# Kernel tuning notes

Hardware: AMD Instinct MI355X
Metric: run time of the kernel (lower is better)

## Reference

```python
import jax, jax.numpy as jnp
import numpy as np

ALPHA = 0.5
MOM = 0.9            # momentum m in the recurrence
ACTIVATION = "tanh"
NUM_LAYERS = 2
CACHE = 32           # GROUP size
NK = 4               # n_kernel_feats
B, N, E = 4, 4096, 128


def _act(T):
    if ACTIVATION == "leaky-relu":
        return jax.nn.leaky_relu(T)
    elif ACTIVATION == "tanh":
        return jnp.tanh(T)
    return T


def _group_indices(N, cache, stage):
    # vectorized group_pos_to_index_v2 over all (group_nr, pos_in_group)
    m = N // cache
    o = np.arange(cache)
    s = 0 if stage == 0 else (1 << (stage - 1)) % m
    g = np.arange(m)[:, None]
    block = (g + o[None, :] * s) % m
    return jnp.asarray(block * cache + o[None, :])  # [m, cache], a permutation of 0..N-1


def _ncn_layer(X, Xa, W, stage):
    B, N, E = X.shape
    ce = E // NK
    m = N // CACHE
    idx = _group_indices(N, CACHE, stage)           # [m, cache]
    Wi = W[:E].reshape(NK, ce)
    Wj = W[E:].reshape(NK, ce)
    # gather groups: [B, m, NK, cache, ce]
    xg = jnp.moveaxis(X.reshape(B, N, NK, ce)[:, idx], 3, 2)
    xag = jnp.moveaxis(Xa.reshape(B, N, NK, ce)[:, idx], 3, 2)

    def step(carry, j):
        xi, xa = carry                               # [B, m, NK, cache, ce]
        xj = jnp.take(xi, j, axis=3)                 # [B, m, NK, ce]  (row start_j)
        sim = (jnp.einsum('bgnke,ne->bgnk', xi, Wi)
               + jnp.einsum('bgne,ne->bgn', xj, Wj)[..., None])   # [B, m, NK, cache]
        T = ALPHA * xi + (1.0 - ALPHA) * sim[..., None] * xj[:, :, :, None, :]
        F = _act(T)
        ya = MOM * xa + (1.0 - MOM) * F
        yi = MOM * xi + (1.0 - MOM) * ya
        return (yi, ya), None

    (yi, ya), _ = jax.lax.scan(step, (xg, xag), jnp.arange(CACHE))

    # scatter back; idx is a permutation so .set reproduces the += into zeros
    def scatter(v):
        v = jnp.moveaxis(v, 2, 3).reshape(B, m * CACHE, E)
        return jnp.zeros((B, N, E), v.dtype).at[:, idx.reshape(-1)].set(v)

    return scatter(yi), scatter(ya)


def setup_inputs() -> dict:
    key = jax.random.key(0)
    k1, k2, k3 = jax.random.split(key, 3)
    x = jax.random.normal(k1, (B, N, E), jnp.float32)
    xa = jax.random.normal(k2, (B, N, E), jnp.float32)
    W = jax.random.normal(k3, (NUM_LAYERS, 2 * E), jnp.float32)
    return {"x": x, "xa": xa, "W": W}


def reference(x, xa, W):
    for l in range(NUM_LAYERS):
        x, xa = _ncn_layer(x, xa, W[l], l)
    return x, xa
```

## Files before the change

kernel.cpp:

```cpp
#include <hip/hip_runtime.h>


namespace {
constexpr int kB = 4;
constexpr int kN = 4096;
constexpr int kE = 128;
constexpr int kCE = 32;
constexpr int kF  = 8;
constexpr int kQ  = kF / 2;
constexpr int kCache = 32;
constexpr int kM = kN / kCache;

typedef __attribute__((ext_vector_type(2))) float f32x2;

__device__ __forceinline__ f32x2 pk_fma(f32x2 a, f32x2 b, f32x2 c) {
    return __builtin_elementwise_fma(a, b, c);
}
}

__global__ void __launch_bounds__(128) ncn_layer_kernel(
    const float* __restrict__ x_in, const float* __restrict__ xa_in,
    const float* __restrict__ Wl,
    float* __restrict__ x_out, float* __restrict__ xa_out,
    int s)
{
    const int blk = blockIdx.x;
    const int n   = blk & 3;
    const int g   = (blk >> 2) & (kM - 1);
    const int b   = blk >> 9;
    const int t   = threadIdx.x;
    const int w   = t >> 6;
    const int l   = t & 63;
    const int orr = l >> 2;
    const int f   = l & 3;
    const int row = w * 16 + orr;

    const int r = (((g + row * s) & (kM - 1)) << 5) + row;
    const size_t base = ((size_t)(b * kN + r)) * kE + n * kCE + f * kF;

    constexpr float L1 = 1.4426950408889634f;

    f32x2 xi[kQ], xa[kQ], wi[kQ], wj[kQ];

    {
        const float4* xi4 = reinterpret_cast<const float4*>(x_in + base);
        const float4* xa4 = reinterpret_cast<const float4*>(xa_in + base);
        const float4* wi4 = reinterpret_cast<const float4*>(Wl + n * kCE + f * kF);
        const float4* wj4 = reinterpret_cast<const float4*>(Wl + kE + n * kCE + f * kF);
#pragma unroll
        for (int q = 0; q < kQ / 2; ++q) {
            float4 v = xi4[q];
            xi[2 * q + 0] = f32x2{v.x, v.y}; xi[2 * q + 1] = f32x2{v.z, v.w};
            float4 a = xa4[q];
            xa[2 * q + 0] = f32x2{a.x, a.y}; xa[2 * q + 1] = f32x2{a.z, a.w};
            float4 u = wi4[q];
            wi[2 * q + 0] = f32x2{u.x * L1, u.y * L1};
            wi[2 * q + 1] = f32x2{u.z * L1, u.w * L1};
            float4 ww = wj4[q];
            wj[2 * q + 0] = f32x2{ww.x * L1, ww.y * L1};
            wj[2 * q + 1] = f32x2{ww.z * L1, ww.w * L1};
        }
    }

    __shared__ float rowbuf[2][kCE];

    if (t < 4) {
        float4* w4 = reinterpret_cast<float4*>(&rowbuf[0][f * kF]);
#pragma unroll
        for (int q = 0; q < kQ / 2; ++q) {
            float4 v;
            v.x = xi[2 * q + 0].x; v.y = xi[2 * q + 0].y;
            v.z = xi[2 * q + 1].x; v.w = xi[2 * q + 1].y;
            w4[q] = v;
        }
    }
    __syncthreads();

#pragma unroll 4
    for (int j = 0; j < kCache; ++j) {
        const int p = j & 1;

        f32x2 xj[kQ];
        {
            const float4* r4 = reinterpret_cast<const float4*>(&rowbuf[p][f * kF]);
#pragma unroll
            for (int q = 0; q < kQ / 2; ++q) {
                float4 v = r4[q];
                xj[2 * q + 0] = f32x2{v.x, v.y};
                xj[2 * q + 1] = f32x2{v.z, v.w};
            }
        }

        f32x2 a01 = xi[0] * wi[0];
        f32x2 a23 = xi[1] * wi[1];
        f32x2 b01 = xj[0] * wj[0];
        f32x2 b23 = xj[1] * wj[1];
        a01 = pk_fma(xi[2], wi[2], a01);
        a23 = pk_fma(xi[3], wi[3], a23);
        b01 = pk_fma(xj[2], wj[2], b01);
        b23 = pk_fma(xj[3], wj[3], b23);
        f32x2 uv = (a01 + a23) + (b01 + b23);
        float u  = uv.x + uv.y;

        u += __shfl_xor(u, 1, 64);
        u += __shfl_xor(u, 2, 64);
        const float sim = u;
        const f32x2 sv  = {sim, sim};
        const f32x2 l12 = {L1, L1};
        const f32x2 one = {1.0f, 1.0f};
        const f32x2 m02 = {-0.2f, -0.2f};
        const f32x2 c9  = {0.9f, 0.9f};
        const f32x2 c01 = {0.1f, 0.1f};

#pragma unroll
        for (int q = 0; q < kQ; ++q) {
            f32x2 arg = pk_fma(xj[q], sv, xi[q] * l12);
            f32x2 t2;
            t2.x = __builtin_amdgcn_exp2f(arg.x);
            t2.y = __builtin_amdgcn_exp2f(arg.y);
            f32x2 den = t2 + one;
            f32x2 rc;
            rc.x = __builtin_amdgcn_rcpf(den.x);
            rc.y = __builtin_amdgcn_rcpf(den.y);
            xa[q] = pk_fma(m02, rc, pk_fma(c9, xa[q], c01));
            xi[q] = pk_fma(c01, xa[q], xi[q] * c9);
        }

        const int nj = (j + 1) & 31;
        if (row == nj) {
            float4* w4 = reinterpret_cast<float4*>(&rowbuf[p ^ 1][f * kF]);
#pragma unroll
            for (int q = 0; q < kQ / 2; ++q) {
                float4 v;
                v.x = xi[2 * q + 0].x; v.y = xi[2 * q + 0].y;
                v.z = xi[2 * q + 1].x; v.w = xi[2 * q + 1].y;
                w4[q] = v;
            }
        }
        __syncthreads();
    }

    {
        float4* xo4 = reinterpret_cast<float4*>(x_out + base);
        float4* ao4 = reinterpret_cast<float4*>(xa_out + base);
#pragma unroll
        for (int q = 0; q < kQ / 2; ++q) {
            float4 v;
            v.x = xi[2 * q + 0].x; v.y = xi[2 * q + 0].y;
            v.z = xi[2 * q + 1].x; v.w = xi[2 * q + 1].y;
            xo4[q] = v;
            float4 a;
            a.x = xa[2 * q + 0].x; a.y = xa[2 * q + 0].y;
            a.z = xa[2 * q + 1].x; a.w = xa[2 * q + 1].y;
            ao4[q] = a;
        }
    }
}

extern "C" void kernel_launch(void* const* d_in, const int* in_sizes, int n_in,
                              void* d_out, int out_size, void* d_ws, size_t ws_size,
                              hipStream_t stream) {
    const float* x  = (const float*)d_in[0];
    const float* xa = (const float*)d_in[1];
    const float* W  = (const float*)d_in[2];

    const size_t plane = (size_t)kB * kN * kE;

    float* x_mid  = (float*)d_ws;
    float* xa_mid = x_mid + plane;

    float* x_out  = (float*)d_out;
    float* xa_out = x_out + plane;

    const dim3 grid(kB * kM * 4);
    const dim3 block(128);

    ncn_layer_kernel<<<grid, block, 0, stream>>>(x, xa, W, x_mid, xa_mid, 0);
    ncn_layer_kernel<<<grid, block, 0, stream>>>(x_mid, xa_mid, W + 2 * kE,
                                                 x_out, xa_out, 1);
}
```

Measured before the change: 119.9 us.

## Map each group to one wavefront and broadcast rows via ds_bpermute

Each (batch, group, kernel-feature) unit now runs in a single 64-lane wavefront, with 2 lanes per row holding 16 features each, instead of 128 threads using shared memory plus a __syncthreads per step. Row j is broadcast with ds_bpermute, the xj·Wj term is taken via readlane from precomputed per-row dot products, and pair sums use DPP. State is kept pre-scaled by log2(e) so the exp2 argument and the momentum updates fold into fewer FMAs. This removes block barriers and LDS round trips from the 32-step serial loop, at the cost of more registers per lane and more bpermute traffic.

Measured after the change: 119.2 us. Within noise of the previous version (-0.6%).

```diff
diff --git a/kernel.cpp b/kernel.cpp
--- a/kernel.cpp
+++ b/kernel.cpp
@@ -6,115 +6,113 @@
 constexpr int kN = 4096;
 constexpr int kE = 128;
 constexpr int kCE = 32;
-constexpr int kF  = 8;
-constexpr int kQ  = kF / 2;
 constexpr int kCache = 32;
 constexpr int kM = kN / kCache;
+
+constexpr float kL1    = 1.4426950408889634f;
+constexpr float kInvL1 = 0.6931471805599453f;
 
 typedef __attribute__((ext_vector_type(2))) float f32x2;
 
 __device__ __forceinline__ f32x2 pk_fma(f32x2 a, f32x2 b, f32x2 c) {
     return __builtin_elementwise_fma(a, b, c);
 }
+
+__device__ __forceinline__ float pair_sum(float x) {
+    int sw = __builtin_amdgcn_update_dpp(0, __float_as_int(x),
+                                         0xB1, 0xF, 0xF, true);
+    return x + __int_as_float(sw);
 }
 
-__global__ void __launch_bounds__(128) ncn_layer_kernel(
+__device__ __forceinline__ f32x2 bperm2(int byte_addr, f32x2 v) {
+    f32x2 r;
+    r.x = __int_as_float(
+        __builtin_amdgcn_ds_bpermute(byte_addr, __float_as_int(v.x)));
+    r.y = __int_as_float(
+        __builtin_amdgcn_ds_bpermute(byte_addr, __float_as_int(v.y)));
+    return r;
+}
+}
+
+__global__ void __launch_bounds__(256, 2) ncn_layer_kernel(
     const float* __restrict__ x_in, const float* __restrict__ xa_in,
     const float* __restrict__ Wl,
     float* __restrict__ x_out, float* __restrict__ xa_out,
     int s)
 {
-    const int blk = blockIdx.x;
-    const int n   = blk & 3;
-    const int g   = (blk >> 2) & (kM - 1);
-    const int b   = blk >> 9;
-    const int t   = threadIdx.x;
-    const int w   = t >> 6;
-    const int l   = t & 63;
-    const int orr = l >> 2;
-    const int f   = l & 3;
-    const int row = w * 16 + orr;
+    const int t    = threadIdx.x;
+    const int wv   = t >> 6;
+    const int l    = t & 63;
+    const int unit = blockIdx.x * 4 + wv;
+    const int n    = unit & 3;
+    const int g    = (unit >> 2) & (kM - 1);
+    const int b    = unit >> 9;
 
-    const int r = (((g + row * s) & (kM - 1)) << 5) + row;
-    const size_t base = ((size_t)(b * kN + r)) * kE + n * kCE + f * kF;
+    const int h = l & 1;
+    const int r = l >> 1;
 
-    constexpr float L1 = 1.4426950408889634f;
+    const int gr = (((g + r * s) & (kM - 1)) << 5) + r;
+    const size_t base = ((size_t)(b * kN + gr)) * kE + n * kCE + h * 16;
 
-    f32x2 xi[kQ], xa[kQ], wi[kQ], wj[kQ];
-
+    f32x2 xi[8], ya[8], wi[8], wj[8];
     {
         const float4* xi4 = reinterpret_cast<const float4*>(x_in + base);
         const float4* xa4 = reinterpret_cast<const float4*>(xa_in + base);
-        const float4* wi4 = reinterpret_cast<const float4*>(Wl + n * kCE + f * kF);
-        const float4* wj4 = reinterpret_cast<const float4*>(Wl + kE + n * kCE + f * kF);
+        const float4* wi4 = reinterpret_cast<const float4*>(Wl + n * kCE + h * 16);
+        const float4* wj4 = reinterpret_cast<const float4*>(Wl + kE + n * kCE + h * 16);
 #pragma unroll
-        for (int q = 0; q < kQ / 2; ++q) {
-            float4 v = xi4[q];
-            xi[2 * q + 0] = f32x2{v.x, v.y}; xi[2 * q + 1] = f32x2{v.z, v.w};
-            float4 a = xa4[q];
-            xa[2 * q + 0] = f32x2{a.x, a.y}; xa[2 * q + 1] = f32x2{a.z, a.w};
-            float4 u = wi4[q];
-            wi[2 * q + 0] = f32x2{u.x * L1, u.y * L1};
-            wi[2 * q + 1] = f32x2{u.z * L1, u.w * L1};
-            float4 ww = wj4[q];
-            wj[2 * q + 0] = f32x2{ww.x * L1, ww.y * L1};
-            wj[2 * q + 1] = f32x2{ww.z * L1, ww.w * L1};
+        for (int q4 = 0; q4 < 4; ++q4) {
+            float4 v = xi4[q4];
+            xi[2 * q4 + 0] = f32x2{v.x * kL1, v.y * kL1};
+            xi[2 * q4 + 1] = f32x2{v.z * kL1, v.w * kL1};
+            float4 a = xa4[q4];
+            ya[2 * q4 + 0] = f32x2{a.x * (0.1f * kL1), a.y * (0.1f * kL1)};
+            ya[2 * q4 + 1] = f32x2{a.z * (0.1f * kL1), a.w * (0.1f * kL1)};
+            float4 u = wi4[q4];
+            wi[2 * q4 + 0] = f32x2{u.x * kInvL1, u.y * kInvL1};
+            wi[2 * q4 + 1] = f32x2{u.z * kInvL1, u.w * kInvL1};
+            float4 w2 = wj4[q4];
+            wj[2 * q4 + 0] = f32x2{w2.x * kInvL1, w2.y * kInvL1};
+            wj[2 * q4 + 1] = f32x2{w2.z * kInvL1, w2.w * kInvL1};
         }
     }
 
-    __shared__ float rowbuf[2][kCE];
+    const int v4h = h << 2;
 
-    if (t < 4) {
-        float4* w4 = reinterpret_cast<float4*>(&rowbuf[0][f * kF]);
-#pragma unroll
-        for (int q = 0; q < kQ / 2; ++q) {
-            float4 v;
-            v.x = xi[2 * q + 0].x; v.y = xi[2 * q + 0].y;
-            v.z = xi[2 * q + 1].x; v.w = xi[2 * q + 1].y;
-            w4[q] = v;
-        }
-    }
-    __syncthreads();
-
-#pragma unroll 4
-    for (int j = 0; j < kCache; ++j) {
-        const int p = j & 1;
-
-        f32x2 xj[kQ];
-        {
-            const float4* r4 = reinterpret_cast<const float4*>(&rowbuf[p][f * kF]);
-#pragma unroll
-            for (int q = 0; q < kQ / 2; ++q) {
-                float4 v = r4[q];
-                xj[2 * q + 0] = f32x2{v.x, v.y};
-                xj[2 * q + 1] = f32x2{v.z, v.w};
-            }
-        }
-
-        f32x2 a01 = xi[0] * wi[0];
-        f32x2 a23 = xi[1] * wi[1];
-        f32x2 b01 = xj[0] * wj[0];
-        f32x2 b23 = xj[1] * wj[1];
-        a01 = pk_fma(xi[2], wi[2], a01);
-        a23 = pk_fma(xi[3], wi[3], a23);
-        b01 = pk_fma(xj[2], wj[2], b01);
-        b23 = pk_fma(xj[3], wj[3], b23);
-        f32x2 uv = (a01 + a23) + (b01 + b23);
-        float u  = uv.x + uv.y;
-
-        u += __shfl_xor(u, 1, 64);
-        u += __shfl_xor(u, 2, 64);
-        const float sim = u;
-        const f32x2 sv  = {sim, sim};
-        const f32x2 l12 = {L1, L1};
-        const f32x2 one = {1.0f, 1.0f};
-        const f32x2 m02 = {-0.2f, -0.2f};
-        const f32x2 c9  = {0.9f, 0.9f};
-        const f32x2 c01 = {0.1f, 0.1f};
+    const f32x2 one = {1.0f, 1.0f};
+    const f32x2 c9  = {0.9f, 0.9f};
+    const f32x2 cA  = {0.01f * kL1, 0.01f * kL1};
+    const f32x2 cB  = {-0.02f * kL1, -0.02f * kL1};
 
 #pragma unroll
-        for (int q = 0; q < kQ; ++q) {
-            f32x2 arg = pk_fma(xj[q], sv, xi[q] * l12);
+    for (int j = 0; j < kCache; ++j) {
+        const int addr = v4h + 8 * j;
+        f32x2 xj[8];
+#pragma unroll
+        for (int q = 0; q < 8; ++q) xj[q] = bperm2(addr, xi[q]);
+
+        f32x2 a0 = xi[0] * wi[0], a1 = xi[1] * wi[1];
+        f32x2 e0 = xi[0] * wj[0], e1 = xi[1] * wj[1];
+        a0 = pk_fma(xi[2], wi[2], a0); a1 = pk_fma(xi[3], wi[3], a1);
+        e0 = pk_fma(xi[2], wj[2], e0); e1 = pk_fma(xi[3], wj[3], e1);
+        a0 = pk_fma(xi[4], wi[4], a0); a1 = pk_fma(xi[5], wi[5], a1);
+        e0 = pk_fma(xi[4], wj[4], e0); e1 = pk_fma(xi[5], wj[5], e1);
+        a0 = pk_fma(xi[6], wi[6], a0); a1 = pk_fma(xi[7], wi[7], a1);
+        e0 = pk_fma(xi[6], wj[6], e0); e1 = pk_fma(xi[7], wj[7], e1);
+        f32x2 av = a0 + a1, ev = e0 + e1;
+        float a = av.x + av.y;
+        float e = ev.x + ev.y;
+        a = pair_sum(a);
+        e = pair_sum(e);
+
+        const float dj = __int_as_float(
+            __builtin_amdgcn_readlane(__float_as_int(e), 2 * j));
+        const float sim = a + dj;
+        const f32x2 sv = {sim, sim};
+
+#pragma unroll
+        for (int q = 0; q < 8; ++q) {
+            f32x2 arg = pk_fma(xj[q], sv, xi[q]);
             f32x2 t2;
             t2.x = __builtin_amdgcn_exp2f(arg.x);
             t2.y = __builtin_amdgcn_exp2f(arg.y);
@@ -122,37 +120,27 @@
             f32x2 rc;
             rc.x = __builtin_amdgcn_rcpf(den.x);
             rc.y = __builtin_amdgcn_rcpf(den.y);
-            xa[q] = pk_fma(m02, rc, pk_fma(c9, xa[q], c01));
-            xi[q] = pk_fma(c01, xa[q], xi[q] * c9);
+            f32x2 yt = pk_fma(ya[q], c9, cA);
+            ya[q] = pk_fma(rc, cB, yt);
+            xi[q] = pk_fma(xi[q], c9, ya[q]);
         }
-
-        const int nj = (j + 1) & 31;
-        if (row == nj) {
-            float4* w4 = reinterpret_cast<float4*>(&rowbuf[p ^ 1][f * kF]);
-#pragma unroll
-            for (int q = 0; q < kQ / 2; ++q) {
-                float4 v;
-                v.x = xi[2 * q + 0].x; v.y = xi[2 * q + 0].y;
-                v.z = xi[2 * q + 1].x; v.w = xi[2 * q + 1].y;
-                w4[q] = v;
-            }
-        }
-        __syncthreads();
     }
 
     {
+        const f32x2 ivx = {kInvL1, kInvL1};
+        const f32x2 iva = {10.0f * kInvL1, 10.0f * kInvL1};
         float4* xo4 = reinterpret_cast<float4*>(x_out + base);
         float4* ao4 = reinterpret_cast<float4*>(xa_out + base);
 #pragma unroll
-        for (int q = 0; q < kQ / 2; ++q) {
-            float4 v;
-            v.x = xi[2 * q + 0].x; v.y = xi[2 * q + 0].y;
-            v.z = xi[2 * q + 1].x; v.w = xi[2 * q + 1].y;
-            xo4[q] = v;
-            float4 a;
-            a.x = xa[2 * q + 0].x; a.y = xa[2 * q + 0].y;
-            a.z = xa[2 * q + 1].x; a.w = xa[2 * q + 1].y;
-            ao4[q] = a;
+        for (int q4 = 0; q4 < 4; ++q4) {
+            f32x2 x0 = xi[2 * q4 + 0] * ivx;
+            f32x2 x1 = xi[2 * q4 + 1] * ivx;
+            float4 v; v.x = x0.x; v.y = x0.y; v.z = x1.x; v.w = x1.y;
+            xo4[q4] = v;
+            f32x2 a0 = ya[2 * q4 + 0] * iva;
+            f32x2 a1 = ya[2 * q4 + 1] * iva;
+            float4 w; w.x = a0.x; w.y = a0.y; w.z = a1.x; w.w = a1.y;
+            ao4[q4] = w;
         }
     }
 }
@@ -172,8 +160,8 @@
     float* x_out  = (float*)d_out;
     float* xa_out = x_out + plane;
 
-    const dim3 grid(kB * kM * 4);
-    const dim3 block(128);
+    const dim3 grid(kB * kM);
+    const dim3 block(256);
 
     ncn_layer_kernel<<<grid, block, 0, stream>>>(x, xa, W, x_mid, xa_mid, 0);
     ncn_layer_kernel<<<grid, block, 0, stream>>>(x_mid, xa_mid, W + 2 * kE,
```
